# Kernel optimization log

Measured on AMD Instinct MI355X. Metric: run time of the kernel, lower is better.

Reference implementation:

```python
import jax, jax.numpy as jnp
from jax import lax
import numpy as np

N_IN, N_REC, N_OUT = 128, 512, 20
N_T, N_B = 1000, 64
THR = 1.0
DT, TAU_M, TAU_O = 1.0, 20.0, 20.0
B_O = 0.0
ALPHA = float(np.exp(-DT / TAU_M))  # membrane decay
KAPPA = float(np.exp(-DT / TAU_O))  # output decay
GAIN = (0.5, 0.1, 0.5)              # w_init_gain


def _kaiming(key, shape, gain):
    fan_in = shape[1]
    std = float(np.sqrt(2.0 / fan_in))
    return gain * std * jax.random.normal(key, shape, dtype=jnp.float32)


def setup_inputs() -> dict:
    key = jax.random.key(0)
    k1, k2, k3, k4, k5 = jax.random.split(key, 5)
    x = jax.random.uniform(k1, (N_B, N_T, N_IN), dtype=jnp.float32)
    yt = jax.random.uniform(k2, (N_B, N_T, N_OUT), dtype=jnp.float32)
    w_in = _kaiming(k3, (N_REC, N_IN), GAIN[0])
    w_rec = _kaiming(k4, (N_REC, N_REC), GAIN[1])
    w_out = _kaiming(k5, (N_OUT, N_REC), GAIN[2])
    return {"x": x, "yt": yt, "w_in": w_in, "w_rec": w_rec, "w_out": w_out}


def reference(x, yt, w_in, w_rec, w_out):
    # zero self-recurrence, as in forward(): w_rec *= (1 - eye)
    w_rec_m = w_rec * (1.0 - jnp.eye(N_REC, dtype=w_rec.dtype))

    def step(carry, x_t):
        v, z, vo = carry  # (n_b, n_rec), (n_b, n_rec), (n_b, n_out)
        v_new = ALPHA * v + z @ w_rec_m.T + x_t @ w_in.T - z * THR
        z_new = (v_new > THR).astype(v_new.dtype)
        vo_new = KAPPA * vo + z_new @ w_out.T + B_O
        return (v_new, z_new, vo_new), vo_new

    v0 = jnp.zeros((N_B, N_REC), dtype=x.dtype)
    z0 = jnp.zeros((N_B, N_REC), dtype=x.dtype)
    vo0 = jnp.zeros((N_B, N_OUT), dtype=x.dtype)
    # loop runs t = 0 .. n_t-2, consuming x[:, t, :]
    xs = jnp.swapaxes(x, 0, 1)[: N_T - 1]  # (n_t-1, n_b, n_in)
    _, vo_traj = lax.scan(step, (v0, z0, vo0), xs)
    vo = jnp.concatenate([vo0[None], vo_traj], axis=0)  # (n_t, n_b, n_out), vo[0]=0
    # classif=True: softmax over output units after permute -> (n_b, n_t, n_out)
    yo = jax.nn.softmax(jnp.swapaxes(vo, 0, 1), axis=2)
    return yo
```

## Files before the change

### kernel.cpp

```cpp
#include <hip/hip_runtime.h>
#include <cstdint>
#include <cstddef>

#define N_IN   128
#define N_REC  512
#define N_OUT  20
#define N_T    1000
#define N_B    64
#define NSTEP  999
#define ALPHA_F 0.95122945308685302734375f
#define KAPPA_F 0.95122945308685302734375f

typedef unsigned long long ull;

#define OFF_WINT   0ull
#define OFF_WRECT  262144ull
#define OFF_ZMASK  1312768ull
#define OFF_U      5404672ull
#define OFF_XPROJ  10519552ull
#define NEED_PRE   (OFF_XPROJ + 130940928ull)

#define SENT_OFF   (512 << 11)

__device__ __forceinline__ void bar_lgkm() {
  asm volatile("s_waitcnt lgkmcnt(0)" ::: "memory");
  __builtin_amdgcn_s_barrier();
}

__global__ __launch_bounds__(256) void k_setup(
    const float* __restrict__ w_in, const float* __restrict__ w_rec,
    float* __restrict__ w_inT, float* __restrict__ w_recT) {
  int idx = blockIdx.x * 256 + threadIdx.x;
  if (idx < N_IN * N_REC) {
    int k = idx >> 9, i = idx & 511;
    w_inT[idx] = w_in[i * N_IN + k];
  } else if (idx < N_IN * N_REC + 513 * N_REC) {
    int r = idx - N_IN * N_REC;
    int j = r >> 9, i = r & 511;
    w_recT[r] = (j < N_REC && i != j) ? w_rec[i * N_REC + j] : 0.0f;
  }
}

#define XROWS 48
__global__ __launch_bounds__(256) void k_xprojE(
    const float* __restrict__ x, const float* __restrict__ w_inT,
    float* __restrict__ xproj) {
  __shared__ float xs[XROWS][N_IN];
  int tid = threadIdx.x;
  int R0 = blockIdx.x * XROWS;
  #pragma unroll
  for (int u = 0; u < 6; ++u) {
    int id = tid + u * 256;
    int rr = id >> 5, c = id & 31;
    int s = R0 + rr;
    int b = s / NSTEP, t = s - b * NSTEP;
    float4 xv = ((const float4*)x)[(size_t)(b * N_T + t) * 32 + c];
    xs[rr][4 * c]     = xv.x;
    xs[rr][4 * c + 1] = xv.y;
    xs[rr][4 * c + 2] = xv.z;
    xs[rr][4 * c + 3] = xv.w;
  }
  __syncthreads();
  float acc[XROWS][2];
  #pragma unroll
  for (int r = 0; r < XROWS; ++r) { acc[r][0] = 0.f; acc[r][1] = 0.f; }
  for (int k = 0; k < N_IN; ++k) {
    float wa = w_inT[k * N_REC + tid];
    float wb = w_inT[k * N_REC + tid + 256];
    #pragma unroll
    for (int r = 0; r < XROWS; ++r) {
      acc[r][0] = fmaf(xs[r][k], wa, acc[r][0]);
      acc[r][1] = fmaf(xs[r][k], wb, acc[r][1]);
    }
  }
  #pragma unroll
  for (int r = 0; r < XROWS; ++r) {
    size_t o0 = (size_t)(R0 + r) * N_REC + tid;
    xproj[o0]       = acc[r][0];
    xproj[o0 + 256] = acc[r][1];
  }
}

struct F16R { float f[16]; };
struct I16  { int4 a, b, c, d; };

__device__ __forceinline__ void iload16(I16& r, const int* __restrict__ L, int base) {
  r.a = *(const int4*)(L + base);
  r.b = *(const int4*)(L + base + 4);
  r.c = *(const int4*)(L + base + 8);
  r.d = *(const int4*)(L + base + 12);
}

__device__ __forceinline__ void gload16i(F16R& r, const I16& I,
                                         const char* __restrict__ wb, int t4) {
  r.f[0]  = *(const float*)(wb + (uint32_t)(I.a.x + t4));
  r.f[1]  = *(const float*)(wb + (uint32_t)(I.a.y + t4));
  r.f[2]  = *(const float*)(wb + (uint32_t)(I.a.z + t4));
  r.f[3]  = *(const float*)(wb + (uint32_t)(I.a.w + t4));
  r.f[4]  = *(const float*)(wb + (uint32_t)(I.b.x + t4));
  r.f[5]  = *(const float*)(wb + (uint32_t)(I.b.y + t4));
  r.f[6]  = *(const float*)(wb + (uint32_t)(I.b.z + t4));
  r.f[7]  = *(const float*)(wb + (uint32_t)(I.b.w + t4));
  r.f[8]  = *(const float*)(wb + (uint32_t)(I.c.x + t4));
  r.f[9]  = *(const float*)(wb + (uint32_t)(I.c.y + t4));
  r.f[10] = *(const float*)(wb + (uint32_t)(I.c.z + t4));
  r.f[11] = *(const float*)(wb + (uint32_t)(I.c.w + t4));
  r.f[12] = *(const float*)(wb + (uint32_t)(I.d.x + t4));
  r.f[13] = *(const float*)(wb + (uint32_t)(I.d.y + t4));
  r.f[14] = *(const float*)(wb + (uint32_t)(I.d.z + t4));
  r.f[15] = *(const float*)(wb + (uint32_t)(I.d.w + t4));
}

__device__ __forceinline__ float add16(float rec, const F16R& r) {
  #pragma unroll
  for (int u = 0; u < 16; ++u) rec = __fadd_rn(rec, r.f[u]);
  return rec;
}

template <bool PRE>
__global__ __launch_bounds__(512) void k_scanE(
    const float* __restrict__ xproj, const float* __restrict__ x,
    const float* __restrict__ w_inT, const float* __restrict__ w_recT,
    ull* __restrict__ zmask) {
  __shared__ __align__(16) int list[2][512];
  __shared__ ull zbuf[2][8];
  __shared__ float xrow[2][N_IN];
  int tid = threadIdx.x, b = blockIdx.x;
  int lane = tid & 63, wave = tid >> 6;
  int t4 = tid << 2;
  const char* wb = (const char*)w_recT;
  float v = 0.f, z = 0.f;
  int nb = 0;
  float xcur = 0.f;
  if (PRE) {
    xcur = xproj[(size_t)(b * NSTEP) * N_REC + tid];
  } else {
    if (tid < N_IN) xrow[0][tid] = x[(size_t)(b * N_T) * N_IN + tid];
  }
  __syncthreads();
  for (int t = 0; t < NSTEP; ++t) {
    int p = t & 1, q = p ^ 1;
    const int* L = list[p];
    float xnext = 0.f;
    if (PRE) {
      if (t + 1 < NSTEP)
        xnext = xproj[(size_t)(b * NSTEP + t + 1) * N_REC + tid];
    } else {
      if (tid < N_IN && t + 1 < NSTEP)
        xrow[(t + 1) & 1][tid] = x[((size_t)b * N_T + t + 1) * N_IN + tid];
    }
    float xin;
    if (PRE) {
      xin = xcur;
    } else {
      xin = 0.f;
      const float* xr = xrow[t & 1];
      for (int k = 0; k < N_IN; ++k)
        xin = fmaf(xr[k], w_inT[k * N_REC + tid], xin);
    }
    float rec = 0.f;
    {
      I16 I0, I1, I2, I3;
      F16R D0, D1, D2, D3;
      if (nb > 0) iload16(I0, L, 0);
      if (nb > 1) iload16(I1, L, 16);
      if (nb > 2) iload16(I2, L, 32);
      if (nb > 0) gload16i(D0, I0, wb, t4);
      if (nb > 1) gload16i(D1, I1, wb, t4);
      if (nb > 2) gload16i(D2, I2, wb, t4);
      if (nb > 3) iload16(I3, L, 48);
      int k = 0;
      while (k < nb) {
        rec = add16(rec, D0);
        if (k + 3 < nb) gload16i(D3, I3, wb, t4);
        if (k + 4 < nb) iload16(I0, L, (k + 4) << 4);
        ++k; if (k >= nb) break;
        rec = add16(rec, D1);
        if (k + 3 < nb) gload16i(D0, I0, wb, t4);
        if (k + 4 < nb) iload16(I1, L, (k + 4) << 4);
        ++k; if (k >= nb) break;
        rec = add16(rec, D2);
        if (k + 3 < nb) gload16i(D1, I1, wb, t4);
        if (k + 4 < nb) iload16(I2, L, (k + 4) << 4);
        ++k; if (k >= nb) break;
        rec = add16(rec, D3);
        if (k + 3 < nb) gload16i(D2, I2, wb, t4);
        if (k + 4 < nb) iload16(I3, L, (k + 4) << 4);
        ++k;
      }
    }
    float t1 = __fmul_rn(ALPHA_F, v);
    t1 = __fadd_rn(t1, rec);
    t1 = __fadd_rn(t1, xin);
    v  = __fsub_rn(t1, z);
    int on = v > 1.0f;
    z = on ? 1.0f : 0.0f;
    ull mask = __ballot(on);
    if (lane == 0) {
      zmask[((size_t)b * NSTEP + t) * 8 + wave] = mask;
      zbuf[q][wave] = mask;
    }
    bar_lgkm();
    int base = 0, ntot = 0;
    #pragma unroll
    for (int w = 0; w < 8; ++w) {
      ull mw = zbuf[q][w];
      int c = __popcll(mw);
      if (w < wave) base += c;
      ntot += c;
    }
    if (on) {
      int pc = __popcll(mask & ((1ull << lane) - 1));
      list[q][base + pc] = tid << 11;
    }
    int np16 = (ntot + 15) & ~15;
    if (tid >= ntot && tid < np16) list[q][tid] = SENT_OFF;
    bar_lgkm();
    nb = np16 >> 4;
    xcur = xnext;
  }
}

__global__ __launch_bounds__(256) void k_U(
    const ull* __restrict__ zmask, const float* __restrict__ w_out,
    float* __restrict__ U) {
  __shared__ float wT[N_REC][N_OUT];
  int tid = threadIdx.x;
  for (int e = tid; e < N_REC * N_OUT; e += 256) {
    int j = e / N_OUT, o = e - j * N_OUT;
    wT[j][o] = w_out[o * N_REC + j];
  }
  __syncthreads();
  int n = blockIdx.x * 256 + tid;
  if (n >= N_B * NSTEP) return;
  ull m[8];
  #pragma unroll
  for (int w = 0; w < 8; ++w) m[w] = zmask[(size_t)n * 8 + w];
  float acc[N_OUT];
  #pragma unroll
  for (int o = 0; o < N_OUT; ++o) acc[o] = 0.f;
  #pragma unroll
  for (int w = 0; w < 8; ++w) {
    ull bits = m[w];
    while (bits) {
      int j = __builtin_ctzll(bits);
      bits &= bits - 1;
      const float4* r4 = (const float4*)&wT[(w << 6) + j][0];
      float4 r0 = r4[0], r1 = r4[1], r2 = r4[2], r3 = r4[3], r4v = r4[4];
      acc[0]  += r0.x;  acc[1]  += r0.y;  acc[2]  += r0.z;  acc[3]  += r0.w;
      acc[4]  += r1.x;  acc[5]  += r1.y;  acc[6]  += r1.z;  acc[7]  += r1.w;
      acc[8]  += r2.x;  acc[9]  += r2.y;  acc[10] += r2.z;  acc[11] += r2.w;
      acc[12] += r3.x;  acc[13] += r3.y;  acc[14] += r3.z;  acc[15] += r3.w;
      acc[16] += r4v.x; acc[17] += r4v.y; acc[18] += r4v.z; acc[19] += r4v.w;
    }
  }
  float4* Up = (float4*)(U + (size_t)n * N_OUT);
  Up[0] = make_float4(acc[0],  acc[1],  acc[2],  acc[3]);
  Up[1] = make_float4(acc[4],  acc[5],  acc[6],  acc[7]);
  Up[2] = make_float4(acc[8],  acc[9],  acc[10], acc[11]);
  Up[3] = make_float4(acc[12], acc[13], acc[14], acc[15]);
  Up[4] = make_float4(acc[16], acc[17], acc[18], acc[19]);
}

__global__ __launch_bounds__(64) void k_voscan(
    const float* __restrict__ U, float* __restrict__ out) {
  int n = blockIdx.x * 64 + threadIdx.x;
  if (n >= N_B * N_OUT) return;
  int b = n / N_OUT, o = n - b * N_OUT;
  out[(size_t)(b * N_T) * N_OUT + o] = 0.f;
  float acc = 0.f;
  #pragma unroll 9
  for (int t = 0; t < NSTEP; ++t) {
    acc = __fadd_rn(__fmul_rn(KAPPA_F, acc),
                    U[(size_t)(b * NSTEP + t) * N_OUT + o]);
    out[(size_t)(b * N_T + t + 1) * N_OUT + o] = acc;
  }
}

__global__ __launch_bounds__(256) void k_softmax(float* __restrict__ out) {
  int n = blockIdx.x * 256 + threadIdx.x;
  if (n >= N_B * N_T) return;
  float* p = out + (size_t)n * N_OUT;
  float vals[N_OUT];
  #pragma unroll
  for (int o = 0; o < N_OUT; ++o) vals[o] = p[o];
  float mx = vals[0];
  #pragma unroll
  for (int o = 1; o < N_OUT; ++o) mx = fmaxf(mx, vals[o]);
  float s = 0.f;
  #pragma unroll
  for (int o = 0; o < N_OUT; ++o) { vals[o] = expf(vals[o] - mx); s += vals[o]; }
  float inv = 1.0f / s;
  #pragma unroll
  for (int o = 0; o < N_OUT; ++o) p[o] = vals[o] * inv;
}

extern "C" void kernel_launch(void* const* d_in, const int* in_sizes, int n_in,
                              void* d_out, int out_size, void* d_ws, size_t ws_size,
                              hipStream_t stream) {
  int ix = -1, iwin = -1, iwrec = -1, iwout = -1;
  for (int i = 0; i < n_in; ++i) {
    long long s = in_sizes[i];
    if (s == (long long)N_B * N_T * N_IN) ix = i;
    else if (s == N_REC * N_IN)  iwin = i;
    else if (s == N_REC * N_REC) iwrec = i;
    else if (s == N_OUT * N_REC) iwout = i;
  }
  if (ix < 0 || iwin < 0 || iwrec < 0 || iwout < 0) {
    if (n_in >= 5) { ix = 0; iwin = 2; iwrec = 3; iwout = 4; }
    else           { ix = 0; iwin = 1; iwrec = 2; iwout = 3; }
  }
  const float* x     = (const float*)d_in[ix];
  const float* w_in  = (const float*)d_in[iwin];
  const float* w_rec = (const float*)d_in[iwrec];
  const float* w_out = (const float*)d_in[iwout];
  float* out = (float*)d_out;
  char* ws = (char*)d_ws;

  float* w_inT  = (float*)(ws + OFF_WINT);
  float* w_recT = (float*)(ws + OFF_WRECT);
  ull*   zmask  = (ull*)(ws + OFF_ZMASK);
  float* U      = (float*)(ws + OFF_U);
  float* xproj  = (float*)(ws + OFF_XPROJ);

  k_setup<<<1282, 256, 0, stream>>>(w_in, w_rec, w_inT, w_recT);
  if (ws_size >= NEED_PRE) {
    k_xprojE<<<1332, 256, 0, stream>>>(x, w_inT, xproj);
    k_scanE<true><<<N_B, 512, 0, stream>>>(xproj, x, w_inT, w_recT, zmask);
  } else {
    k_scanE<false><<<N_B, 512, 0, stream>>>(xproj, x, w_inT, w_recT, zmask);
  }
  k_U<<<250, 256, 0, stream>>>(zmask, w_out, U);
  k_voscan<<<20, 64, 0, stream>>>(U, out);
  k_softmax<<<250, 256, 0, stream>>>(out);
}
```

Before: 2.277 ms.

## Issue a fixed 128-entry gather batch per step and prefetch input projection two steps ahead

The recurrent gather loop is restructured so every step issues eight 16-entry index loads and eight weight gathers up front, with the spike list padded with sentinel entries to at least 128. Any spikes beyond 128 fall back to a serial loop. This replaces the four-deep rotating software pipeline with one large batch of independent loads to raise memory-level parallelism. The xproj prefetch now runs two steps ahead, and launch bounds request two blocks per CU. The cost is wasted sentinel gathers when few neurons spike, higher register pressure from holding eight batches at once, and an unpipelined tail when many spike.

```diff
diff --git a/kernel.cpp b/kernel.cpp
--- a/kernel.cpp
+++ b/kernel.cpp
@@ -118,7 +118,7 @@
 }
 
 template <bool PRE>
-__global__ __launch_bounds__(512) void k_scanE(
+__global__ __launch_bounds__(512, 2) void k_scanE(
     const float* __restrict__ xproj, const float* __restrict__ x,
     const float* __restrict__ w_inT, const float* __restrict__ w_recT,
     ull* __restrict__ zmask) {
@@ -130,21 +130,23 @@
   int t4 = tid << 2;
   const char* wb = (const char*)w_recT;
   float v = 0.f, z = 0.f;
-  int nb = 0;
-  float xcur = 0.f;
+  int nbt = 0;
+  float xcur = 0.f, xn1 = 0.f;
   if (PRE) {
     xcur = xproj[(size_t)(b * NSTEP) * N_REC + tid];
+    if (NSTEP > 1) xn1 = xproj[(size_t)(b * NSTEP + 1) * N_REC + tid];
   } else {
     if (tid < N_IN) xrow[0][tid] = x[(size_t)(b * N_T) * N_IN + tid];
   }
+  list[0][tid] = SENT_OFF;
   __syncthreads();
   for (int t = 0; t < NSTEP; ++t) {
     int p = t & 1, q = p ^ 1;
     const int* L = list[p];
-    float xnext = 0.f;
+    float xn2 = 0.f;
     if (PRE) {
-      if (t + 1 < NSTEP)
-        xnext = xproj[(size_t)(b * NSTEP + t + 1) * N_REC + tid];
+      if (t + 2 < NSTEP)
+        xn2 = xproj[(size_t)(b * NSTEP + t + 2) * N_REC + tid];
     } else {
       if (tid < N_IN && t + 1 < NSTEP)
         xrow[(t + 1) & 1][tid] = x[((size_t)b * N_T + t + 1) * N_IN + tid];
@@ -160,33 +162,19 @@
     }
     float rec = 0.f;
     {
-      I16 I0, I1, I2, I3;
-      F16R D0, D1, D2, D3;
-      if (nb > 0) iload16(I0, L, 0);
-      if (nb > 1) iload16(I1, L, 16);
-      if (nb > 2) iload16(I2, L, 32);
-      if (nb > 0) gload16i(D0, I0, wb, t4);
-      if (nb > 1) gload16i(D1, I1, wb, t4);
-      if (nb > 2) gload16i(D2, I2, wb, t4);
-      if (nb > 3) iload16(I3, L, 48);
-      int k = 0;
-      while (k < nb) {
-        rec = add16(rec, D0);
-        if (k + 3 < nb) gload16i(D3, I3, wb, t4);
-        if (k + 4 < nb) iload16(I0, L, (k + 4) << 4);
-        ++k; if (k >= nb) break;
-        rec = add16(rec, D1);
-        if (k + 3 < nb) gload16i(D0, I0, wb, t4);
-        if (k + 4 < nb) iload16(I1, L, (k + 4) << 4);
-        ++k; if (k >= nb) break;
-        rec = add16(rec, D2);
-        if (k + 3 < nb) gload16i(D1, I1, wb, t4);
-        if (k + 4 < nb) iload16(I2, L, (k + 4) << 4);
-        ++k; if (k >= nb) break;
-        rec = add16(rec, D3);
-        if (k + 3 < nb) gload16i(D2, I2, wb, t4);
-        if (k + 4 < nb) iload16(I3, L, (k + 4) << 4);
-        ++k;
+      I16 I[8];
+      F16R D[8];
+      #pragma unroll
+      for (int k = 0; k < 8; ++k) iload16(I[k], L, k << 4);
+      #pragma unroll
+      for (int k = 0; k < 8; ++k) gload16i(D[k], I[k], wb, t4);
+      #pragma unroll
+      for (int k = 0; k < 8; ++k) rec = add16(rec, D[k]);
+      for (int k = 8; k < nbt; ++k) {
+        I16 It; F16R Dt;
+        iload16(It, L, k << 4);
+        gload16i(Dt, It, wb, t4);
+        rec = add16(rec, Dt);
       }
     }
     float t1 = __fmul_rn(ALPHA_F, v);
@@ -214,10 +202,11 @@
       list[q][base + pc] = tid << 11;
     }
     int np16 = (ntot + 15) & ~15;
-    if (tid >= ntot && tid < np16) list[q][tid] = SENT_OFF;
+    int pad_end = np16 > 128 ? np16 : 128;
+    if (tid >= ntot && tid < pad_end) list[q][tid] = SENT_OFF;
     bar_lgkm();
-    nb = np16 >> 4;
-    xcur = xnext;
+    nbt = np16 > 128 ? (np16 >> 4) : 8;
+    xcur = xn1; xn1 = xn2;
   }
 }
 
```

New measurement: 3.256 ms. +43.0%, slower.
